# Kernel optimization log

Hardware: AMD Instinct MI355X
Metric: run time of the kernel (lower is better)

## Reference

```python
import jax, jax.numpy as jnp
import numpy as np

TEMPERATURE = 0.07
EPS = 1e-12  # F.normalize eps


def setup_inputs() -> dict:
    key = jax.random.key(0)
    k1, k2, k3 = jax.random.split(key, 3)
    B, D, N_CLASSES = 4096, 256, 1000
    return {
        "z_i": jax.random.normal(k1, (B, D), dtype=jnp.float32),
        "z_j": jax.random.normal(k2, (B, D), dtype=jnp.float32),
        "labels": jax.random.randint(k3, (B,), 0, N_CLASSES, dtype=jnp.int64),
    }


def _l2_normalize(x):
    norm = jnp.sqrt(jnp.sum(x * x, axis=1, keepdims=True))
    return x / jnp.maximum(norm, EPS)


def reference(z_i, z_j, labels):
    zi = _l2_normalize(z_i)
    zj = _l2_normalize(z_j)
    z = jnp.concatenate([zi, zj], axis=0)          # (2B, D)
    lab = jnp.concatenate([labels, labels], axis=0)  # (2B,)
    N = z.shape[0]

    sim = jnp.matmul(z, z.T) / TEMPERATURE          # (2B, 2B)

    eye = jnp.eye(N, dtype=bool)
    same = lab[:, None] == lab[None, :]
    pos_mask = same & ~eye                          # positives: same label, not self
    neg_mask = ~same                                # negatives: different label

    # pos_sim_i = sum of similarities over positives (a sum, per original code)
    pos_sim = jnp.sum(jnp.where(pos_mask, sim, 0.0), axis=1)  # (2B,)
    # log(neg_sim_i) = logsumexp over negatives (stable, same math as sum of exp)
    lse_neg = jax.nn.logsumexp(jnp.where(neg_mask, sim, -jnp.inf), axis=1)
    # -log(exp(p) / (exp(p) + n)) = log(1 + exp(log n - p))
    loss_i = jnp.logaddexp(0.0, lse_neg - pos_sim)  # (2B,)

    has_pos = jnp.any(pos_mask, axis=1)
    loss = jnp.sum(jnp.where(has_pos, loss_i, 0.0)) / N
    return loss
```

## Files before the change

kernel.cpp:

```cpp
#include <hip/hip_runtime.h>

#define NROWS 8192
#define BQ    4096
#define DDIM  256
#define NSLC  32
#define INV_T (1.0f/0.07f)
#define K2EXP (1.4426950408889634f/0.07f)

typedef short bf16x8 __attribute__((ext_vector_type(8)));
typedef float f32x4  __attribute__((ext_vector_type(4)));
typedef unsigned short u16;

__device__ __forceinline__ u16 f2bf(float f) {
  unsigned u = __float_as_uint(f);
  u += 0x7fffu + ((u >> 16) & 1u);
  return (u16)(u >> 16);
}

__global__ void norm_cast_kernel(const float* __restrict__ zi,
                                 const float* __restrict__ zj,
                                 u16* __restrict__ zb,
                                 float* __restrict__ out) {
  if (blockIdx.x == 0 && threadIdx.x == 0) *out = 0.0f;
  int wave = threadIdx.x >> 6;
  int lane = threadIdx.x & 63;
  int row  = blockIdx.x * 4 + wave;
  const float* src = (row < BQ) ? (zi + (size_t)row * DDIM)
                                : (zj + (size_t)(row - BQ) * DDIM);
  float4 v = ((const float4*)src)[lane];
  float s = v.x*v.x + v.y*v.y + v.z*v.z + v.w*v.w;
  #pragma unroll
  for (int m = 32; m; m >>= 1) s += __shfl_xor(s, m, 64);
  float scale = 1.0f / fmaxf(sqrtf(s), 1e-12f);
  ushort4 o;
  o.x = f2bf(v.x * scale); o.y = f2bf(v.y * scale);
  o.z = f2bf(v.z * scale); o.w = f2bf(v.w * scale);
  ((ushort4*)(zb + (size_t)row * DDIM))[lane] = o;
}

#define GL2LDS(gp, lp) \
  __builtin_amdgcn_global_load_lds((__attribute__((address_space(1))) void*)(gp), \
                                   (__attribute__((address_space(3))) void*)(lp), 16, 0, 0)

__global__ __launch_bounds__(256) void simloss_kernel(
    const u16* __restrict__ zb, const int* __restrict__ labels,
    float* __restrict__ pos_p, float* __restrict__ neg_p) {
  __shared__ __align__(16) u16 lsA[128 * 32];
  __shared__ __align__(16) u16 lsB[128 * 32];

  const int tid  = threadIdx.x;
  const int w    = tid >> 6;
  const int lane = tid & 63;
  const int ln   = lane & 15;
  const int qd   = lane >> 4;
  const int wr   = w >> 1;
  const int wc   = w & 1;
  const int r0   = blockIdx.x * 128;
  const int cb   = blockIdx.y * 512;

  const int strow = lane >> 2;
  const int slot  = lane & 3;
  const int stk   = (slot ^ ((strow >> 1) & 3)) * 8;
  const int rdsw  = (ln >> 1) & 3;

  int rowidx[16], rowlab[16];
  #pragma unroll
  for (int ri = 0; ri < 4; ++ri)
    #pragma unroll
    for (int r = 0; r < 4; ++r) {
      int slt = ri * 4 + r;
      int row = r0 + wr * 64 + ri * 16 + qd * 4 + r;
      rowidx[slt] = row;
      rowlab[slt] = labels[row & (BQ - 1)];
    }

  float posA[16], negA[16];
  #pragma unroll
  for (int i = 0; i < 16; ++i) { posA[i] = 0.0f; negA[i] = 0.0f; }

  for (int ci = 0; ci < 4; ++ci) {
    const int c0 = cb + ci * 128;
    int colv[4], clab[4];
    #pragma unroll
    for (int mi = 0; mi < 4; ++mi) {
      colv[mi] = c0 + wc * 64 + mi * 16 + ln;
      clab[mi] = labels[colv[mi] & (BQ - 1)];
    }

    const f32x4 z4 = {0.f, 0.f, 0.f, 0.f};
    f32x4 acc[4][4];
    #pragma unroll
    for (int ri = 0; ri < 4; ++ri)
      #pragma unroll
      for (int mi = 0; mi < 4; ++mi) acc[ri][mi] = z4;

    for (int kk = 0; kk < 8; ++kk) {
      const int k0 = kk * 32;
      #pragma unroll
      for (int j = 0; j < 2; ++j) {
        int rbase = w * 32 + j * 16;
        const u16* ga = zb + (size_t)(r0 + rbase + strow) * DDIM + k0 + stk;
        GL2LDS(ga, &lsA[rbase * 32]);
        const u16* gb = zb + (size_t)(c0 + rbase + strow) * DDIM + k0 + stk;
        GL2LDS(gb, &lsB[rbase * 32]);
      }
      __syncthreads();

      bf16x8 av[4], bv[4];
      #pragma unroll
      for (int ri = 0; ri < 4; ++ri)
        av[ri] = *(const bf16x8*)&lsA[(wr * 64 + ri * 16 + ln) * 32 + (qd ^ rdsw) * 8];
      #pragma unroll
      for (int mi = 0; mi < 4; ++mi)
        bv[mi] = *(const bf16x8*)&lsB[(wc * 64 + mi * 16 + ln) * 32 + (qd ^ rdsw) * 8];
      #pragma unroll
      for (int ri = 0; ri < 4; ++ri)
        #pragma unroll
        for (int mi = 0; mi < 4; ++mi)
          acc[ri][mi] = __builtin_amdgcn_mfma_f32_16x16x32_bf16(
              av[ri], bv[mi], acc[ri][mi], 0, 0, 0);
      __syncthreads();
    }

    #pragma unroll
    for (int ri = 0; ri < 4; ++ri)
      #pragma unroll
      for (int mi = 0; mi < 4; ++mi) {
        f32x4 v = acc[ri][mi];
        #pragma unroll
        for (int r = 0; r < 4; ++r) {
          int slt = ri * 4 + r;
          float s = v[r];
          bool same = (rowlab[slt] == clab[mi]);
          bool diag = (rowidx[slt] == colv[mi]);
          posA[slt] += (same && !diag) ? s : 0.0f;
          negA[slt] += same ? 0.0f : __builtin_amdgcn_exp2f(s * K2EXP);
        }
      }
  }

  #pragma unroll
  for (int i = 0; i < 16; ++i) {
    #pragma unroll
    for (int m = 1; m < 16; m <<= 1) {
      posA[i] += __shfl_xor(posA[i], m, 64);
      negA[i] += __shfl_xor(negA[i], m, 64);
    }
  }
  if (ln == 0) {
    int s = blockIdx.y * 2 + wc;
    #pragma unroll
    for (int i = 0; i < 16; ++i) {
      pos_p[(size_t)s * NROWS + rowidx[i]] = posA[i];
      neg_p[(size_t)s * NROWS + rowidx[i]] = negA[i];
    }
  }
}

__global__ void loss_kernel(const float* __restrict__ pos_p,
                            const float* __restrict__ neg_p,
                            float* __restrict__ out) {
  int row = blockIdx.x * 256 + threadIdx.x;
  float p = 0.0f, n = 0.0f;
  #pragma unroll
  for (int s = 0; s < NSLC; ++s) {
    p += pos_p[(size_t)s * NROWS + row];
    n += neg_p[(size_t)s * NROWS + row];
  }
  float l = log1pf(expf(logf(n) - p * INV_T));
  #pragma unroll
  for (int m = 32; m; m >>= 1) l += __shfl_xor(l, m, 64);
  __shared__ float red[4];
  if ((threadIdx.x & 63) == 0) red[threadIdx.x >> 6] = l;
  __syncthreads();
  if (threadIdx.x == 0) {
    float tot = red[0] + red[1] + red[2] + red[3];
    atomicAdd(out, tot * (1.0f / NROWS));
  }
}

extern "C" void kernel_launch(void* const* d_in, const int* in_sizes, int n_in,
                              void* d_out, int out_size, void* d_ws, size_t ws_size,
                              hipStream_t stream) {
  const float* zi     = (const float*)d_in[0];
  const float* zj     = (const float*)d_in[1];
  const int*   labels = (const int*)d_in[2];
  float*       out    = (float*)d_out;

  char* w = (char*)d_ws;
  u16*   zb    = (u16*)w;
  float* pos_p = (float*)(w + (size_t)NROWS * DDIM * sizeof(u16));
  float* neg_p = pos_p + NSLC * NROWS;

  hipLaunchKernelGGL(norm_cast_kernel, dim3(2048), dim3(256), 0, stream,
                     zi, zj, zb, out);
  hipLaunchKernelGGL(simloss_kernel, dim3(64, 16), dim3(256), 0, stream,
                     zb, labels, pos_p, neg_p);
  hipLaunchKernelGGL(loss_kernel, dim3(32), dim3(256), 0, stream,
                     pos_p, neg_p, out);
}
```

Measured before the change: 134.9 us.

## Exploit similarity symmetry: compute upper-triangular tiles only with atomic row/column accumulation

Since the similarity matrix is symmetric, the kernel now launches one block per upper-triangular 128x128 tile pair (2080 tiles instead of 4096). Each off-diagonal tile adds its positive sums and negative exp-sums both to its rows and, through cross-lane shuffles, to its columns. Diagonal tiles keep the masked self-exclusion. Per-slice partial buffers are replaced by global atomic accumulators that are zeroed in the normalization kernel, which also makes the final loss kernel a single read per row. The aim is to halve the MFMA and exp work, at the cost of many float atomics and nondeterministic summation order.

```diff
diff --git a/kernel.cpp b/kernel.cpp
--- a/kernel.cpp
+++ b/kernel.cpp
@@ -3,7 +3,6 @@
 #define NROWS 8192
 #define BQ    4096
 #define DDIM  256
-#define NSLC  32
 #define INV_T (1.0f/0.07f)
 #define K2EXP (1.4426950408889634f/0.07f)
 
@@ -20,8 +19,10 @@
 __global__ void norm_cast_kernel(const float* __restrict__ zi,
                                  const float* __restrict__ zj,
                                  u16* __restrict__ zb,
+                                 float* __restrict__ posneg,
                                  float* __restrict__ out) {
   if (blockIdx.x == 0 && threadIdx.x == 0) *out = 0.0f;
+  if (blockIdx.x < 64) posneg[blockIdx.x * 256 + threadIdx.x] = 0.0f;
   int wave = threadIdx.x >> 6;
   int lane = threadIdx.x & 63;
   int row  = blockIdx.x * 4 + wave;
@@ -44,7 +45,7 @@
 
 __global__ __launch_bounds__(256) void simloss_kernel(
     const u16* __restrict__ zb, const int* __restrict__ labels,
-    float* __restrict__ pos_p, float* __restrict__ neg_p) {
+    float* __restrict__ pos, float* __restrict__ neg) {
   __shared__ __align__(16) u16 lsA[128 * 32];
   __shared__ __align__(16) u16 lsB[128 * 32];
 
@@ -55,8 +56,14 @@
   const int qd   = lane >> 4;
   const int wr   = w >> 1;
   const int wc   = w & 1;
-  const int r0   = blockIdx.x * 128;
-  const int cb   = blockIdx.y * 512;
+
+  const int u = blockIdx.x;
+  int rb = (int)((129.0f - sqrtf((float)(16641 - 8 * u))) * 0.5f);
+  while ((rb + 1) * (129 - (rb + 1)) / 2 <= u) ++rb;
+  while (rb * (129 - rb) / 2 > u) --rb;
+  const int cbk = rb + (u - rb * (129 - rb) / 2);
+  const int r0 = rb * 128;
+  const int c0 = cbk * 128;
 
   const int strow = lane >> 2;
   const int slot  = lane & 3;
@@ -73,55 +80,53 @@
       rowidx[slt] = row;
       rowlab[slt] = labels[row & (BQ - 1)];
     }
+  int colv[4], clab[4];
+  #pragma unroll
+  for (int mi = 0; mi < 4; ++mi) {
+    colv[mi] = c0 + wc * 64 + mi * 16 + ln;
+    clab[mi] = labels[colv[mi] & (BQ - 1)];
+  }
+
+  const f32x4 z4 = {0.f, 0.f, 0.f, 0.f};
+  f32x4 acc[4][4];
+  #pragma unroll
+  for (int ri = 0; ri < 4; ++ri)
+    #pragma unroll
+    for (int mi = 0; mi < 4; ++mi) acc[ri][mi] = z4;
+
+  for (int kk = 0; kk < 8; ++kk) {
+    const int k0 = kk * 32;
+    #pragma unroll
+    for (int j = 0; j < 2; ++j) {
+      int rbase = w * 32 + j * 16;
+      const u16* ga = zb + (size_t)(r0 + rbase + strow) * DDIM + k0 + stk;
+      GL2LDS(ga, &lsA[rbase * 32]);
+      const u16* gb = zb + (size_t)(c0 + rbase + strow) * DDIM + k0 + stk;
+      GL2LDS(gb, &lsB[rbase * 32]);
+    }
+    __syncthreads();
+
+    bf16x8 av[4], bv[4];
+    #pragma unroll
+    for (int ri = 0; ri < 4; ++ri)
+      av[ri] = *(const bf16x8*)&lsA[(wr * 64 + ri * 16 + ln) * 32 + (qd ^ rdsw) * 8];
+    #pragma unroll
+    for (int mi = 0; mi < 4; ++mi)
+      bv[mi] = *(const bf16x8*)&lsB[(wc * 64 + mi * 16 + ln) * 32 + (qd ^ rdsw) * 8];
+    #pragma unroll
+    for (int ri = 0; ri < 4; ++ri)
+      #pragma unroll
+      for (int mi = 0; mi < 4; ++mi)
+        acc[ri][mi] = __builtin_amdgcn_mfma_f32_16x16x32_bf16(
+            av[ri], bv[mi], acc[ri][mi], 0, 0, 0);
+    __syncthreads();
+  }
 
   float posA[16], negA[16];
   #pragma unroll
   for (int i = 0; i < 16; ++i) { posA[i] = 0.0f; negA[i] = 0.0f; }
 
-  for (int ci = 0; ci < 4; ++ci) {
-    const int c0 = cb + ci * 128;
-    int colv[4], clab[4];
-    #pragma unroll
-    for (int mi = 0; mi < 4; ++mi) {
-      colv[mi] = c0 + wc * 64 + mi * 16 + ln;
-      clab[mi] = labels[colv[mi] & (BQ - 1)];
-    }
-
-    const f32x4 z4 = {0.f, 0.f, 0.f, 0.f};
-    f32x4 acc[4][4];
-    #pragma unroll
-    for (int ri = 0; ri < 4; ++ri)
-      #pragma unroll
-      for (int mi = 0; mi < 4; ++mi) acc[ri][mi] = z4;
-
-    for (int kk = 0; kk < 8; ++kk) {
-      const int k0 = kk * 32;
-      #pragma unroll
-      for (int j = 0; j < 2; ++j) {
-        int rbase = w * 32 + j * 16;
-        const u16* ga = zb + (size_t)(r0 + rbase + strow) * DDIM + k0 + stk;
-        GL2LDS(ga, &lsA[rbase * 32]);
-        const u16* gb = zb + (size_t)(c0 + rbase + strow) * DDIM + k0 + stk;
-        GL2LDS(gb, &lsB[rbase * 32]);
-      }
-      __syncthreads();
-
-      bf16x8 av[4], bv[4];
-      #pragma unroll
-      for (int ri = 0; ri < 4; ++ri)
-        av[ri] = *(const bf16x8*)&lsA[(wr * 64 + ri * 16 + ln) * 32 + (qd ^ rdsw) * 8];
-      #pragma unroll
-      for (int mi = 0; mi < 4; ++mi)
-        bv[mi] = *(const bf16x8*)&lsB[(wc * 64 + mi * 16 + ln) * 32 + (qd ^ rdsw) * 8];
-      #pragma unroll
-      for (int ri = 0; ri < 4; ++ri)
-        #pragma unroll
-        for (int mi = 0; mi < 4; ++mi)
-          acc[ri][mi] = __builtin_amdgcn_mfma_f32_16x16x32_bf16(
-              av[ri], bv[mi], acc[ri][mi], 0, 0, 0);
-      __syncthreads();
-    }
-
+  if (rb == cbk) {
     #pragma unroll
     for (int ri = 0; ri < 4; ++ri)
       #pragma unroll
@@ -137,6 +142,40 @@
           negA[slt] += same ? 0.0f : __builtin_amdgcn_exp2f(s * K2EXP);
         }
       }
+  } else {
+    float cpos[4], cneg[4];
+    #pragma unroll
+    for (int mi = 0; mi < 4; ++mi) { cpos[mi] = 0.0f; cneg[mi] = 0.0f; }
+    #pragma unroll
+    for (int ri = 0; ri < 4; ++ri)
+      #pragma unroll
+      for (int mi = 0; mi < 4; ++mi) {
+        f32x4 v = acc[ri][mi];
+        #pragma unroll
+        for (int r = 0; r < 4; ++r) {
+          int slt = ri * 4 + r;
+          float s = v[r];
+          bool same = (rowlab[slt] == clab[mi]);
+          float e = same ? 0.0f : __builtin_amdgcn_exp2f(s * K2EXP);
+          float p = same ? s : 0.0f;
+          posA[slt] += p;  negA[slt] += e;
+          cpos[mi]  += p;  cneg[mi]  += e;
+        }
+      }
+    #pragma unroll
+    for (int mi = 0; mi < 4; ++mi) {
+      cpos[mi] += __shfl_xor(cpos[mi], 16, 64);
+      cpos[mi] += __shfl_xor(cpos[mi], 32, 64);
+      cneg[mi] += __shfl_xor(cneg[mi], 16, 64);
+      cneg[mi] += __shfl_xor(cneg[mi], 32, 64);
+    }
+    if (qd == 0) {
+      #pragma unroll
+      for (int mi = 0; mi < 4; ++mi) {
+        atomicAdd(&pos[colv[mi]], cpos[mi]);
+        atomicAdd(&neg[colv[mi]], cneg[mi]);
+      }
+    }
   }
 
   #pragma unroll
@@ -148,25 +187,20 @@
     }
   }
   if (ln == 0) {
-    int s = blockIdx.y * 2 + wc;
     #pragma unroll
     for (int i = 0; i < 16; ++i) {
-      pos_p[(size_t)s * NROWS + rowidx[i]] = posA[i];
-      neg_p[(size_t)s * NROWS + rowidx[i]] = negA[i];
-    }
-  }
-}
-
-__global__ void loss_kernel(const float* __restrict__ pos_p,
-                            const float* __restrict__ neg_p,
+      atomicAdd(&pos[rowidx[i]], posA[i]);
+      atomicAdd(&neg[rowidx[i]], negA[i]);
+    }
+  }
+}
+
+__global__ void loss_kernel(const float* __restrict__ pos,
+                            const float* __restrict__ neg,
                             float* __restrict__ out) {
   int row = blockIdx.x * 256 + threadIdx.x;
-  float p = 0.0f, n = 0.0f;
-  #pragma unroll
-  for (int s = 0; s < NSLC; ++s) {
-    p += pos_p[(size_t)s * NROWS + row];
-    n += neg_p[(size_t)s * NROWS + row];
-  }
+  float p = pos[row];
+  float n = neg[row];
   float l = log1pf(expf(logf(n) - p * INV_T));
   #pragma unroll
   for (int m = 32; m; m >>= 1) l += __shfl_xor(l, m, 64);
@@ -188,14 +222,14 @@
   float*       out    = (float*)d_out;
 
   char* w = (char*)d_ws;
-  u16*   zb    = (u16*)w;
-  float* pos_p = (float*)(w + (size_t)NROWS * DDIM * sizeof(u16));
-  float* neg_p = pos_p + NSLC * NROWS;
+  u16*   zb  = (u16*)w;
+  float* pos = (float*)(w + (size_t)NROWS * DDIM * sizeof(u16));
+  float* neg = pos + NROWS;
 
   hipLaunchKernelGGL(norm_cast_kernel, dim3(2048), dim3(256), 0, stream,
-                     zi, zj, zb, out);
-  hipLaunchKernelGGL(simloss_kernel, dim3(64, 16), dim3(256), 0, stream,
-                     zb, labels, pos_p, neg_p);
+                     zi, zj, zb, pos, out);
+  hipLaunchKernelGGL(simloss_kernel, dim3(2080), dim3(256), 0, stream,
+                     zb, labels, pos, neg);
   hipLaunchKernelGGL(loss_kernel, dim3(32), dim3(256), 0, stream,
-                     pos_p, neg_p, out);
-}
+                     pos, neg, out);
+}
```

New measurement: 141.0 us. 4.5% more time.

## Exploit symmetry of similarity matrix: compute upper-triangular tiles only

Applied to the files above, without the earlier changes.

The similarity kernel now walks only the upper-triangular 128x128 tiles (2080 tiles, 4 per block across 520 blocks), decoding tile coordinates from a linear index. Each tile's results feed both the row partial sums and, for off-diagonal tiles, the column partial sums, so roughly half the matmul and exp work is removed. The partial buffers grow to 256 slices, which the cast kernel zero-fills and the loss kernel reads with smaller blocks. The trade is extra memory traffic for the larger partial arrays and zero-fill, plus additional cross-lane reductions per tile.

```diff
diff --git a/kernel.cpp b/kernel.cpp
--- a/kernel.cpp
+++ b/kernel.cpp
@@ -3,7 +3,7 @@
 #define NROWS 8192
 #define BQ    4096
 #define DDIM  256
-#define NSLC  32
+#define NSLC  256
 #define INV_T (1.0f/0.07f)
 #define K2EXP (1.4426950408889634f/0.07f)
 
@@ -20,8 +20,15 @@
 __global__ void norm_cast_kernel(const float* __restrict__ zi,
                                  const float* __restrict__ zj,
                                  u16* __restrict__ zb,
+                                 float* __restrict__ partials,
                                  float* __restrict__ out) {
   if (blockIdx.x == 0 && threadIdx.x == 0) *out = 0.0f;
+  {
+    unsigned gid = blockIdx.x * 256 + threadIdx.x;
+    #pragma unroll
+    for (int i = 0; i < 8; ++i)
+      partials[(size_t)i * 524288 + gid] = 0.0f;
+  }
   int wave = threadIdx.x >> 6;
   int lane = threadIdx.x & 63;
   int row  = blockIdx.x * 4 + wave;
@@ -55,37 +62,34 @@
   const int qd   = lane >> 4;
   const int wr   = w >> 1;
   const int wc   = w & 1;
-  const int r0   = blockIdx.x * 128;
-  const int cb   = blockIdx.y * 512;
 
   const int strow = lane >> 2;
   const int slot  = lane & 3;
   const int stk   = (slot ^ ((strow >> 1) & 3)) * 8;
   const int rdsw  = (ln >> 1) & 3;
 
-  int rowidx[16], rowlab[16];
-  #pragma unroll
-  for (int ri = 0; ri < 4; ++ri)
-    #pragma unroll
-    for (int r = 0; r < 4; ++r) {
-      int slt = ri * 4 + r;
-      int row = r0 + wr * 64 + ri * 16 + qd * 4 + r;
-      rowidx[slt] = row;
-      rowlab[slt] = labels[row & (BQ - 1)];
-    }
-
-  float posA[16], negA[16];
-  #pragma unroll
-  for (int i = 0; i < 16; ++i) { posA[i] = 0.0f; negA[i] = 0.0f; }
-
-  for (int ci = 0; ci < 4; ++ci) {
-    const int c0 = cb + ci * 128;
-    int colv[4], clab[4];
-    #pragma unroll
-    for (int mi = 0; mi < 4; ++mi) {
-      colv[mi] = c0 + wc * 64 + mi * 16 + ln;
-      clab[mi] = labels[colv[mi] & (BQ - 1)];
-    }
+  #pragma unroll 1
+  for (int t = 0; t < 4; ++t) {
+    const int u = blockIdx.x * 4 + t;
+    int rb = (int)((129.0f - sqrtf((float)(16641 - 8 * u))) * 0.5f);
+    while ((rb + 1) * (129 - (rb + 1)) / 2 <= u) ++rb;
+    while (rb * (129 - rb) / 2 > u) --rb;
+    const int c  = rb + (u - rb * (129 - rb) / 2);
+    const int r0 = rb * 128;
+    const int c0 = c * 128;
+    const bool isdiag = (rb == c);
+
+    int rowlab[16], clab[4];
+    #pragma unroll
+    for (int ri = 0; ri < 4; ++ri)
+      #pragma unroll
+      for (int r = 0; r < 4; ++r) {
+        int row = r0 + wr * 64 + ri * 16 + qd * 4 + r;
+        rowlab[ri * 4 + r] = labels[row & (BQ - 1)];
+      }
+    #pragma unroll
+    for (int mi = 0; mi < 4; ++mi)
+      clab[mi] = labels[(c0 + wc * 64 + mi * 16 + ln) & (BQ - 1)];
 
     const f32x4 z4 = {0.f, 0.f, 0.f, 0.f};
     f32x4 acc[4][4];
@@ -121,6 +125,12 @@
               av[ri], bv[mi], acc[ri][mi], 0, 0, 0);
       __syncthreads();
     }
+
+    float rp[16], rn[16], cp[4], cn[4];
+    #pragma unroll
+    for (int i = 0; i < 16; ++i) { rp[i] = 0.0f; rn[i] = 0.0f; }
+    #pragma unroll
+    for (int mi = 0; mi < 4; ++mi) { cp[mi] = 0.0f; cn[mi] = 0.0f; }
 
     #pragma unroll
     for (int ri = 0; ri < 4; ++ri)
@@ -132,27 +142,49 @@
           int slt = ri * 4 + r;
           float s = v[r];
           bool same = (rowlab[slt] == clab[mi]);
-          bool diag = (rowidx[slt] == colv[mi]);
-          posA[slt] += (same && !diag) ? s : 0.0f;
-          negA[slt] += same ? 0.0f : __builtin_amdgcn_exp2f(s * K2EXP);
+          bool diag = isdiag && (wr == wc) && (ri == mi) && (ln == qd * 4 + r);
+          float e = same ? 0.0f : __builtin_amdgcn_exp2f(s * K2EXP);
+          float p = (same && !diag) ? s : 0.0f;
+          rp[slt] += p;  rn[slt] += e;
+          cp[mi]  += p;  cn[mi]  += e;
         }
       }
-  }
-
-  #pragma unroll
-  for (int i = 0; i < 16; ++i) {
-    #pragma unroll
-    for (int m = 1; m < 16; m <<= 1) {
-      posA[i] += __shfl_xor(posA[i], m, 64);
-      negA[i] += __shfl_xor(negA[i], m, 64);
-    }
-  }
-  if (ln == 0) {
-    int s = blockIdx.y * 2 + wc;
+
     #pragma unroll
     for (int i = 0; i < 16; ++i) {
-      pos_p[(size_t)s * NROWS + rowidx[i]] = posA[i];
-      neg_p[(size_t)s * NROWS + rowidx[i]] = negA[i];
+      #pragma unroll
+      for (int m = 1; m < 16; m <<= 1) {
+        rp[i] += __shfl_xor(rp[i], m, 64);
+        rn[i] += __shfl_xor(rn[i], m, 64);
+      }
+    }
+    if (ln == 0) {
+      const size_t srs = (size_t)(2 * c + wc) * NROWS;
+      #pragma unroll
+      for (int i = 0; i < 16; ++i) {
+        int row = r0 + wr * 64 + (i >> 2) * 16 + qd * 4 + (i & 3);
+        pos_p[srs + row] = rp[i];
+        neg_p[srs + row] = rn[i];
+      }
+    }
+
+    if (!isdiag) {
+      #pragma unroll
+      for (int mi = 0; mi < 4; ++mi) {
+        cp[mi] += __shfl_xor(cp[mi], 16, 64);
+        cp[mi] += __shfl_xor(cp[mi], 32, 64);
+        cn[mi] += __shfl_xor(cn[mi], 16, 64);
+        cn[mi] += __shfl_xor(cn[mi], 32, 64);
+      }
+      if (qd == 0) {
+        const size_t scs = (size_t)(128 + 2 * rb + wr) * NROWS;
+        #pragma unroll
+        for (int mi = 0; mi < 4; ++mi) {
+          int col = c0 + wc * 64 + mi * 16 + ln;
+          pos_p[scs + col] = cp[mi];
+          neg_p[scs + col] = cn[mi];
+        }
+      }
     }
   }
 }
@@ -160,9 +192,9 @@
 __global__ void loss_kernel(const float* __restrict__ pos_p,
                             const float* __restrict__ neg_p,
                             float* __restrict__ out) {
-  int row = blockIdx.x * 256 + threadIdx.x;
+  int row = blockIdx.x * 64 + threadIdx.x;
   float p = 0.0f, n = 0.0f;
-  #pragma unroll
+  #pragma unroll 8
   for (int s = 0; s < NSLC; ++s) {
     p += pos_p[(size_t)s * NROWS + row];
     n += neg_p[(size_t)s * NROWS + row];
@@ -170,13 +202,7 @@
   float l = log1pf(expf(logf(n) - p * INV_T));
   #pragma unroll
   for (int m = 32; m; m >>= 1) l += __shfl_xor(l, m, 64);
-  __shared__ float red[4];
-  if ((threadIdx.x & 63) == 0) red[threadIdx.x >> 6] = l;
-  __syncthreads();
-  if (threadIdx.x == 0) {
-    float tot = red[0] + red[1] + red[2] + red[3];
-    atomicAdd(out, tot * (1.0f / NROWS));
-  }
+  if (threadIdx.x == 0) atomicAdd(out, l * (1.0f / NROWS));
 }
 
 extern "C" void kernel_launch(void* const* d_in, const int* in_sizes, int n_in,
@@ -190,12 +216,12 @@
   char* w = (char*)d_ws;
   u16*   zb    = (u16*)w;
   float* pos_p = (float*)(w + (size_t)NROWS * DDIM * sizeof(u16));
-  float* neg_p = pos_p + NSLC * NROWS;
+  float* neg_p = pos_p + (size_t)NSLC * NROWS;
 
   hipLaunchKernelGGL(norm_cast_kernel, dim3(2048), dim3(256), 0, stream,
-                     zi, zj, zb, out);
-  hipLaunchKernelGGL(simloss_kernel, dim3(64, 16), dim3(256), 0, stream,
+                     zi, zj, zb, pos_p, out);
+  hipLaunchKernelGGL(simloss_kernel, dim3(520), dim3(256), 0, stream,
                      zb, labels, pos_p, neg_p);
-  hipLaunchKernelGGL(loss_kernel, dim3(32), dim3(256), 0, stream,
+  hipLaunchKernelGGL(loss_kernel, dim3(128), dim3(64), 0, stream,
                      pos_p, neg_p, out);
 }
```

After: 170.9 us. 1.27x slower.
